# Kernel tuning notes

Measured on AMD Instinct MI355X. Metric: run time of the kernel, lower is better.

## Reference

```python
import jax, jax.numpy as jnp
import numpy as np

NUM_EMBEDDINGS = 512
EMBEDDING_DIM = 64
COMMITMENT_COST = 0.25


def setup_inputs() -> dict:
    key = jax.random.key(0)
    k1, k2 = jax.random.split(key)
    inputs = jax.random.normal(k1, (64, 32, 32, EMBEDDING_DIM), dtype=jnp.float32)
    # codebook initialized uniform(-1/K, 1/K) as in the torch module
    codebook = jax.random.uniform(
        k2, (NUM_EMBEDDINGS, EMBEDDING_DIM), dtype=jnp.float32,
        minval=-1.0 / NUM_EMBEDDINGS, maxval=1.0 / NUM_EMBEDDINGS)
    return {"inputs": inputs, "codebook": codebook}


def reference(inputs, codebook):
    D = codebook.shape[1]
    K = codebook.shape[0]
    flat = inputs.reshape(-1, D)  # [N, D]
    distances = (jnp.sum(flat * flat, axis=1, keepdims=True)
                 + jnp.sum(codebook * codebook, axis=1)
                 - 2.0 * jnp.matmul(flat, codebook.T))
    idx = jnp.argmin(distances, axis=1)  # [N]
    # direct gather == one-hot @ codebook
    quantized = codebook[idx].reshape(inputs.shape)
    e_latent_loss = jnp.mean((jax.lax.stop_gradient(quantized) - inputs) ** 2)
    q_latent_loss = jnp.mean((quantized - jax.lax.stop_gradient(inputs)) ** 2)
    loss = q_latent_loss + COMMITMENT_COST * e_latent_loss
    # straight-through estimator
    quantized_st = inputs + jax.lax.stop_gradient(quantized - inputs)
    # avg_probs = mean over N of one-hot encodings == normalized bincount
    counts = jnp.zeros((K,), dtype=jnp.float32).at[idx].add(1.0)
    avg_probs = counts / flat.shape[0]
    perplexity = jnp.exp(-jnp.sum(avg_probs * jnp.log(avg_probs + 1e-10)))
    return (quantized_st, loss, perplexity)
```

## Files before the change

kernel.cpp:

```cpp
#include <hip/hip_runtime.h>
#include <stdint.h>


#define VQ_N 65536
#define VQ_D 64
#define VQ_K 512
#define HIST_BLOCKS 32

typedef __attribute__((ext_vector_type(4))) float f32x4;
typedef __attribute__((ext_vector_type(8))) short bf16x8;

__device__ __forceinline__ unsigned short f2bf(float f) {
    unsigned b = __float_as_uint(f);
    return (unsigned short)((b + 0x7fffu + ((b >> 16) & 1u)) >> 16);
}

__global__ __launch_bounds__(512, 4) void vq_fused(const float* __restrict__ x,
                                                   const float* __restrict__ cb,
                                                   float* __restrict__ out,
                                                   int* __restrict__ idx_out,
                                                   float* __restrict__ loss_part) {
    __shared__ unsigned short ldsB[32768];
    __shared__ float lds_se[VQ_K];
    __shared__ int sbestk[128];
    __shared__ float wsum[8];
    const bf16x8* ldsV = reinterpret_cast<const bf16x8*>(ldsB);

    int t = threadIdx.x;
    int w = t >> 6, l = t & 63;
    int lr = l & 15, lg = l >> 4;
    int rowbase = blockIdx.x * 128 + w * 16;

    bf16x8 Ah[2];
    float sq;
    {
        float part = 0.0f;
#pragma unroll
        for (int kt = 0; kt < 2; ++kt) {
            const float4* p = reinterpret_cast<const float4*>(
                x + (size_t)(rowbase + lr) * VQ_D + kt * 32 + lg * 8);
            float4 v0 = p[0], v1 = p[1];
            float vv[8] = {v0.x, v0.y, v0.z, v0.w, v1.x, v1.y, v1.z, v1.w};
            bf16x8 h;
#pragma unroll
            for (int j = 0; j < 8; ++j) {
                h[j] = (short)f2bf(-2.0f * vv[j]);
                part = fmaf(vv[j], vv[j], part);
            }
            Ah[kt] = h;
        }
        part += __shfl_xor(part, 16);
        part += __shfl_xor(part, 32);
        sq = part;
    }

#pragma unroll
    for (int i = 0; i < 8; ++i) {
        int e = i * 512 + t;
        int lane = e & 63, kt = (e >> 6) & 1, ct = e >> 7;
        int col = ct * 16 + (lane & 15);
        int k0 = kt * 32 + (lane >> 4) * 8;
        const float4* p = reinterpret_cast<const float4*>(cb + col * VQ_D + k0);
        float4 v0 = p[0], v1 = p[1];
        float vv[8] = {v0.x, v0.y, v0.z, v0.w, v1.x, v1.y, v1.z, v1.w};
        bf16x8 h;
#pragma unroll
        for (int j = 0; j < 8; ++j) h[j] = (short)f2bf(vv[j]);
        reinterpret_cast<bf16x8*>(ldsB)[e] = h;
    }
    {
        const float4* row = reinterpret_cast<const float4*>(cb + t * VQ_D);
        float s = 0.0f;
#pragma unroll
        for (int i = 0; i < VQ_D / 4; ++i) {
            float4 v = row[i];
            s += v.x * v.x + v.y * v.y + v.z * v.z + v.w * v.w;
        }
        lds_se[t] = s;
    }

    __syncthreads();

    float bd[4];
    int bc[4];
#pragma unroll
    for (int j = 0; j < 4; ++j) {
        bd[j] = 3.4e38f;
        bc[j] = 0;
    }
#pragma unroll
    for (int ct2 = 0; ct2 < 32; ++ct2) {
        int col = ct2 * 16 + lr;
        float se = lds_se[col];
        bf16x8 b0 = ldsV[ct2 * 128 + l];
        bf16x8 b1 = ldsV[ct2 * 128 + 64 + l];
        f32x4 a0 = {se, se, se, se};
        a0 = __builtin_amdgcn_mfma_f32_16x16x32_bf16(Ah[0], b0, a0, 0, 0, 0);
        a0 = __builtin_amdgcn_mfma_f32_16x16x32_bf16(Ah[1], b1, a0, 0, 0, 0);
#pragma unroll
        for (int j = 0; j < 4; ++j) {
            if (a0[j] < bd[j]) {
                bd[j] = a0[j];
                bc[j] = col;
            }
        }
    }

    float dacc = 0.0f;
#pragma unroll
    for (int j = 0; j < 4; ++j) {
        float d = bd[j];
        int cc = bc[j];
#pragma unroll
        for (int off = 1; off <= 8; off <<= 1) {
            float od = __shfl_xor(d, off);
            int oc = __shfl_xor(cc, off);
            if (od < d || (od == d && oc < cc)) {
                d = od;
                cc = oc;
            }
        }
        if (lr == 0) {
            int rloc = w * 16 + lg * 4 + j;
            sbestk[rloc] = cc;
            idx_out[blockIdx.x * 128 + rloc] = cc;
            dacc += d;
        }
    }

    float contrib = dacc + (lg == 0 ? sq : 0.0f);
#pragma unroll
    for (int off = 32; off; off >>= 1) contrib += __shfl_down(contrib, off);
    if (l == 0) wsum[w] = contrib;
    __syncthreads();
    if (t == 0) {
        float s = 0.0f;
#pragma unroll
        for (int i = 0; i < 8; ++i) s += wsum[i];
        loss_part[blockIdx.x] = s;
    }

    {
        int r = t >> 2, q = t & 3;
        int k = sbestk[r];
        const float4* src =
            reinterpret_cast<const float4*>(cb + (size_t)k * VQ_D + q * 16);
        float4* dst = reinterpret_cast<float4*>(
            out + ((size_t)blockIdx.x * 128 + r) * VQ_D + q * 16);
#pragma unroll
        for (int i = 0; i < 4; ++i) dst[i] = src[i];
    }
}

__global__ __launch_bounds__(256) void vq_hist(const int* __restrict__ idx,
                                               unsigned* __restrict__ partial) {
    __shared__ unsigned h[VQ_K];
    int t = threadIdx.x;
    h[t] = 0u;
    h[t + 256] = 0u;
    __syncthreads();
    int base = blockIdx.x * (VQ_N / HIST_BLOCKS) + t;
#pragma unroll
    for (int i = 0; i < VQ_N / HIST_BLOCKS / 256; ++i)
        atomicAdd(&h[idx[base + i * 256]], 1u);
    __syncthreads();
    partial[blockIdx.x * VQ_K + t] = h[t];
    partial[blockIdx.x * VQ_K + t + 256] = h[t + 256];
}

__global__ void vq_final(const unsigned* __restrict__ partial,
                         const float* __restrict__ loss_part,
                         float* __restrict__ out_tail) {
    int t = threadIdx.x;
    unsigned cnt = 0;
#pragma unroll
    for (int b = 0; b < HIST_BLOCKS; ++b) cnt += partial[b * VQ_K + t];
    float p = (float)cnt * (1.0f / (float)VQ_N);
    float term = p * logf(p + 1e-10f);
    float ls = loss_part[t];
#pragma unroll
    for (int off = 32; off; off >>= 1) {
        term += __shfl_down(term, off);
        ls += __shfl_down(ls, off);
    }
    __shared__ float wsH[8], wsL[8];
    int wave = t >> 6, lane = t & 63;
    if (lane == 0) {
        wsH[wave] = term;
        wsL[wave] = ls;
    }
    __syncthreads();
    if (t == 0) {
        float H = 0.0f, L = 0.0f;
#pragma unroll
        for (int i = 0; i < 8; ++i) {
            H += wsH[i];
            L += wsL[i];
        }
        out_tail[0] = L * (1.25f / (float)(VQ_N * VQ_D));
        out_tail[1] = expf(-H);
    }
}

extern "C" void kernel_launch(void* const* d_in, const int* in_sizes, int n_in,
                              void* d_out, int out_size, void* d_ws, size_t ws_size,
                              hipStream_t stream) {
    const float* x = (const float*)d_in[0];
    const float* cb = (const float*)d_in[1];
    float* out = (float*)d_out;

    int* idx = (int*)d_ws;
    float* loss_part = (float*)((char*)d_ws + (VQ_N * 4));
    unsigned* partial = (unsigned*)((char*)loss_part + 2048);

    vq_fused<<<VQ_N / 128, 512, 0, stream>>>(x, cb, out, idx, loss_part);
    vq_hist<<<HIST_BLOCKS, 256, 0, stream>>>(idx, partial);
    vq_final<<<1, 512, 0, stream>>>(partial, loss_part, out + (size_t)VQ_N * VQ_D);
}
```

Measured before the change: 40.66 us.

## Precompute bf16 codebook fragments once and stream them into LDS directly

Adds a small prep kernel that converts the codebook to bf16 MFMA fragment order and computes the codebook squared norms once, writing both to workspace. Each main block then copies the prepared fragments into LDS with global_load_lds DMA instead of having every one of the 512 blocks redo the fp32 load, conversion and norm reduction. This cuts redundant per-block ALU and global traffic and frees registers. In exchange it adds an extra kernel launch and a dependency on workspace layout, and the direct-to-LDS load relies on the per-wave contiguous 16-byte placement being correct.

```diff
diff --git a/kernel.cpp b/kernel.cpp
--- a/kernel.cpp
+++ b/kernel.cpp
@@ -15,8 +15,45 @@
     return (unsigned short)((b + 0x7fffu + ((b >> 16) & 1u)) >> 16);
 }
 
+__device__ __forceinline__ void gld_lds16(const void* g, void* l) {
+    __builtin_amdgcn_global_load_lds(
+        (const __attribute__((address_space(1))) void*)g,
+        (__attribute__((address_space(3))) void*)(uintptr_t)(
+            (char*)l - (char*)nullptr),
+        16, 0, 0);
+}
+
+__global__ __launch_bounds__(256) void vq_prep(const float* __restrict__ cb,
+                                               unsigned short* __restrict__ Bfrag,
+                                               float* __restrict__ sq_e) {
+    int g = blockIdx.x * 256 + threadIdx.x;
+    int lane = g & 63, kt = (g >> 6) & 1, ct = g >> 7;
+    int col = ct * 16 + (lane & 15);
+    int k0 = kt * 32 + (lane >> 4) * 8;
+    const float4* p = reinterpret_cast<const float4*>(cb + (size_t)col * VQ_D + k0);
+    float4 v0 = p[0], v1 = p[1];
+    float vv[8] = {v0.x, v0.y, v0.z, v0.w, v1.x, v1.y, v1.z, v1.w};
+    bf16x8 h;
+#pragma unroll
+    for (int j = 0; j < 8; ++j) h[j] = (short)f2bf(vv[j]);
+    reinterpret_cast<bf16x8*>(Bfrag)[(size_t)(ct * 2 + kt) * 64 + lane] = h;
+
+    if (g < VQ_K) {
+        const float4* row = reinterpret_cast<const float4*>(cb + (size_t)g * VQ_D);
+        float s = 0.0f;
+#pragma unroll
+        for (int i = 0; i < VQ_D / 4; ++i) {
+            float4 v = row[i];
+            s += v.x * v.x + v.y * v.y + v.z * v.z + v.w * v.w;
+        }
+        sq_e[g] = s;
+    }
+}
+
 __global__ __launch_bounds__(512, 4) void vq_fused(const float* __restrict__ x,
+                                                   const unsigned short* __restrict__ Bfrag,
                                                    const float* __restrict__ cb,
+                                                   const float* __restrict__ sq_e,
                                                    float* __restrict__ out,
                                                    int* __restrict__ idx_out,
                                                    float* __restrict__ loss_part) {
@@ -31,6 +68,13 @@
     int lr = l & 15, lg = l >> 4;
     int rowbase = blockIdx.x * 128 + w * 16;
 
+#pragma unroll
+    for (int i = 0; i < 8; ++i) {
+        int e0 = i * 512 + w * 64;
+        gld_lds16(Bfrag + ((size_t)e0 + l) * 8, (void*)&ldsB[e0 * 8]);
+    }
+    lds_se[t] = sq_e[t];
+
     bf16x8 Ah[2];
     float sq;
     {
@@ -52,31 +96,6 @@
         part += __shfl_xor(part, 16);
         part += __shfl_xor(part, 32);
         sq = part;
-    }
-
-#pragma unroll
-    for (int i = 0; i < 8; ++i) {
-        int e = i * 512 + t;
-        int lane = e & 63, kt = (e >> 6) & 1, ct = e >> 7;
-        int col = ct * 16 + (lane & 15);
-        int k0 = kt * 32 + (lane >> 4) * 8;
-        const float4* p = reinterpret_cast<const float4*>(cb + col * VQ_D + k0);
-        float4 v0 = p[0], v1 = p[1];
-        float vv[8] = {v0.x, v0.y, v0.z, v0.w, v1.x, v1.y, v1.z, v1.w};
-        bf16x8 h;
-#pragma unroll
-        for (int j = 0; j < 8; ++j) h[j] = (short)f2bf(vv[j]);
-        reinterpret_cast<bf16x8*>(ldsB)[e] = h;
-    }
-    {
-        const float4* row = reinterpret_cast<const float4*>(cb + t * VQ_D);
-        float s = 0.0f;
-#pragma unroll
-        for (int i = 0; i < VQ_D / 4; ++i) {
-            float4 v = row[i];
-            s += v.x * v.x + v.y * v.y + v.z * v.z + v.w * v.w;
-        }
-        lds_se[t] = s;
     }
 
     __syncthreads();
@@ -209,11 +228,14 @@
     const float* cb = (const float*)d_in[1];
     float* out = (float*)d_out;
 
-    int* idx = (int*)d_ws;
-    float* loss_part = (float*)((char*)d_ws + (VQ_N * 4));
+    unsigned short* Bfrag = (unsigned short*)d_ws;
+    float* sq_e = (float*)((char*)d_ws + (64 << 10));
+    int* idx = (int*)((char*)d_ws + (66 << 10));
+    float* loss_part = (float*)((char*)idx + VQ_N * 4);
     unsigned* partial = (unsigned*)((char*)loss_part + 2048);
 
-    vq_fused<<<VQ_N / 128, 512, 0, stream>>>(x, cb, out, idx, loss_part);
+    vq_prep<<<16, 256, 0, stream>>>(cb, Bfrag, sq_e);
+    vq_fused<<<VQ_N / 128, 512, 0, stream>>>(x, Bfrag, cb, sq_e, out, idx, loss_part);
     vq_hist<<<HIST_BLOCKS, 256, 0, stream>>>(idx, partial);
     vq_final<<<1, 512, 0, stream>>>(partial, loss_part, out + (size_t)VQ_N * VQ_D);
 }
```

New measurement: 32.65 us. -19.7%, faster.
